# Performance work log

Measured on AMD Instinct MI355X. Metric: run time of the kernel, lower is better.

## Reference

```python
import jax, jax.numpy as jnp
import numpy as np

N_NODES = 50000
N_EDGES = 800000
D_IN = 128
D_OUT = 128
BN_EPS = 1e-5


def setup_inputs() -> dict:
    key = jax.random.key(0)
    ks = jax.random.split(key, 8)
    node_feats = jax.random.normal(ks[0], (N_NODES, D_IN), dtype=jnp.float32)
    src = jax.random.randint(ks[1], (N_EDGES,), 0, N_NODES, dtype=jnp.int32)
    dst = jax.random.randint(ks[2], (N_EDGES,), 0, N_NODES, dtype=jnp.int32)
    # Glorot-ish init for weights
    scale = 1.0 / np.sqrt(D_IN)
    W = jax.random.normal(ks[3], (D_IN, D_OUT), dtype=jnp.float32) * scale
    b = jnp.zeros((D_OUT,), dtype=jnp.float32)
    Wr = jax.random.normal(ks[4], (D_IN, D_OUT), dtype=jnp.float32) * scale
    br = jnp.zeros((D_OUT,), dtype=jnp.float32)
    gamma = jnp.ones((D_OUT,), dtype=jnp.float32)
    beta = jnp.zeros((D_OUT,), dtype=jnp.float32)
    return {"node_feats": node_feats, "src": src, "dst": dst, "W": W, "b": b,
            "Wr": Wr, "br": br, "gamma": gamma, "beta": beta}


def reference(node_feats, src, dst, W, b, Wr, br, gamma, beta):
    N = node_feats.shape[0]
    ones_e = jnp.ones(src.shape[0], dtype=node_feats.dtype)
    # DGL GraphConv norm='both': D_out^{-1/2} on source side, D_in^{-1/2} on dest side
    deg_out = jnp.clip(jax.ops.segment_sum(ones_e, src, num_segments=N), 1.0)
    deg_in = jnp.clip(jax.ops.segment_sum(ones_e, dst, num_segments=N), 1.0)
    h = node_feats * jax.lax.rsqrt(deg_out)[:, None]        # [N, D_in]
    agg = jax.ops.segment_sum(h[src], dst, num_segments=N)  # gather + scatter-add, [N, D_in]
    agg = agg * jax.lax.rsqrt(deg_in)[:, None]
    gcn = jax.nn.relu(agg @ W + b)                           # GraphConv activation=relu
    res = jax.nn.relu(node_feats @ Wr + br)                  # residual branch
    y = gcn + res
    # BatchNorm1d (training mode: biased batch stats)
    mean = jnp.mean(y, axis=0)
    var = jnp.mean(jnp.square(y - mean), axis=0)
    out = (y - mean) * jax.lax.rsqrt(var + BN_EPS) * gamma + beta
    return out
```

## Files before the change

kernel.cpp:

```cpp
#include <hip/hip_runtime.h>

#define N_NODES 50000
#define N_EDGES 800000
#define D 128
#define BN_EPS 1e-5f
#define AGG_BLOCKS 2048
#define CHUNKS 64
#define EPC (N_EDGES / CHUNKS)
#define EPC4 (EPC / 4)
#define QUART_BINS 12800
#define QUART_U32 6400
#define NB_MERGE 100
#define NB_PER_Q 25

typedef short bf16x8 __attribute__((ext_vector_type(8)));
typedef float f32x4  __attribute__((ext_vector_type(4)));
typedef float f32x2  __attribute__((ext_vector_type(2)));
typedef unsigned int u32x4 __attribute__((ext_vector_type(4)));
typedef int i32x4 __attribute__((ext_vector_type(4)));


__device__ __forceinline__ unsigned int pack_rne(float a, float b) {
    unsigned int ua = __float_as_uint(a); ua += 0x7fffu + ((ua >> 16) & 1u);
    unsigned int ub = __float_as_uint(b); ub += 0x7fffu + ((ub >> 16) & 1u);
    return (ua >> 16) | (ub & 0xffff0000u);
}
__device__ __forceinline__ unsigned short pack1_rne(float a) {
    unsigned int ua = __float_as_uint(a); ua += 0x7fffu + ((ua >> 16) & 1u);
    return (unsigned short)(ua >> 16);
}
__device__ __forceinline__ unsigned char pack1_fp8(float a) {
    unsigned int u = __builtin_amdgcn_cvt_pk_fp8_f32(a, a, 0, false);
    return (unsigned char)(u & 0xffu);
}

__device__ __forceinline__ void scan_blksum(const int* __restrict__ blk_sum,
                                            int* sh, int t) {
    int v = (t < NB_MERGE) ? blk_sum[t] : 0;
    if (t < 256) sh[t] = v;
    __syncthreads();
    int inc = v;
    #pragma unroll
    for (int off = 1; off < 256; off <<= 1) {
        int u = (t >= off && t < 256) ? sh[t - off] : 0;
        __syncthreads();
        inc += u;
        if (t < 256) sh[t] = inc;
        __syncthreads();
    }
}
#define BLK_OFF(sh, mb) ((mb) ? (sh)[(mb) - 1] : 0)

__global__ __launch_bounds__(256) void hist_kernel(
        const int* __restrict__ dst, const int* __restrict__ src,
        unsigned int* __restrict__ histD, unsigned int* __restrict__ histS,
        const float* __restrict__ W, const float* __restrict__ Wr,
        uint4* __restrict__ pW, uint4* __restrict__ pWr) {
    __shared__ unsigned int h[QUART_U32];
    int tid = threadIdx.x;
    int c = blockIdx.x, r = blockIdx.y;
    if (c >= CHUNKS) {
        if (r != 0 || blockIdx.z != 0) return;
        int t = (c - CHUNKS) * 256 + tid;
        const float* S = (t & 2048) ? Wr : W;
        uint4* Dst     = (t & 2048) ? pWr : pW;
        int e = t & 2047;
        int lane = e & 63, ks = (e >> 6) & 3, ct = e >> 8;
        int n  = ct * 16 + (lane & 15);
        int k0 = ks * 32 + (lane >> 4) * 8;
        float v[8];
        #pragma unroll
        for (int j = 0; j < 8; j++) v[j] = S[(k0 + j) * D + n];
        uint4 rr;
        rr.x = pack_rne(v[0], v[1]); rr.y = pack_rne(v[2], v[3]);
        rr.z = pack_rne(v[4], v[5]); rr.w = pack_rne(v[6], v[7]);
        Dst[e] = rr;
        return;
    }
    const int* keys = blockIdx.z ? src : dst;
    unsigned int* hist = blockIdx.z ? histS : histD;
    for (int j = tid; j < QUART_U32; j += 256) h[j] = 0u;
    __syncthreads();
    int lo = r * QUART_BINS;
    const i32x4* keys4 = (const i32x4*)(keys + c * EPC);
    for (int i = tid; i < EPC4; i += 256) {
        i32x4 k = __builtin_nontemporal_load(keys4 + i);
        int b0 = k.x - lo, b1 = k.y - lo, b2 = k.z - lo, b3 = k.w - lo;
        if ((unsigned)b0 < (unsigned)QUART_BINS) atomicAdd(&h[b0 >> 1], 1u << ((b0 & 1) * 16));
        if ((unsigned)b1 < (unsigned)QUART_BINS) atomicAdd(&h[b1 >> 1], 1u << ((b1 & 1) * 16));
        if ((unsigned)b2 < (unsigned)QUART_BINS) atomicAdd(&h[b2 >> 1], 1u << ((b2 & 1) * 16));
        if ((unsigned)b3 < (unsigned)QUART_BINS) atomicAdd(&h[b3 >> 1], 1u << ((b3 & 1) * 16));
    }
    __syncthreads();
    unsigned int* out = hist + ((size_t)(r * CHUNKS + c)) * QUART_U32;
    for (int j = tid; j < QUART_U32; j += 256) out[j] = h[j];
}

__global__ __launch_bounds__(256) void merge_kernel(
        unsigned int* __restrict__ histD, unsigned int* __restrict__ histS,
        int* __restrict__ cnt_in, int* __restrict__ cnt_out,
        int* __restrict__ row_ptr, int* __restrict__ blk_sum) {
    __shared__ int sh[256];
    int t = threadIdx.x;
    int bx = blockIdx.x;
    int r = bx / NB_PER_Q;
    int q = (bx % NB_PER_Q) * 256 + t;
    int n0 = bx * 512 + t * 2;
    if (blockIdx.y) {
        size_t base = (size_t)r * CHUNKS * QUART_U32 + q;
        unsigned int vals[CHUNKS];
        #pragma unroll
        for (int c = 0; c < CHUNKS; c++)
            vals[c] = histS[base + (size_t)c * QUART_U32];
        unsigned int lo = 0, hi = 0;
        #pragma unroll
        for (int c = 0; c < CHUNKS; c++) {
            lo += vals[c] & 0xffffu; hi += vals[c] >> 16;
        }
        cnt_out[n0]     = (int)lo;
        cnt_out[n0 + 1] = (int)hi;
        return;
    }
    size_t base = (size_t)r * CHUNKS * QUART_U32 + q;
    unsigned int vals[CHUNKS];
    #pragma unroll
    for (int c = 0; c < CHUNKS; c++)
        vals[c] = histD[base + (size_t)c * QUART_U32];
    unsigned int lo = 0, hi = 0;
    #pragma unroll
    for (int c = 0; c < CHUNKS; c++) {
        unsigned int v = vals[c];
        histD[base + (size_t)c * QUART_U32] = lo | (hi << 16);
        lo += v & 0xffffu; hi += v >> 16;
    }
    cnt_in[n0]     = (int)lo;
    cnt_in[n0 + 1] = (int)hi;
    int pair = (int)lo + (int)hi;
    sh[t] = pair;
    __syncthreads();
    int inc = pair;
    #pragma unroll
    for (int off = 1; off < 256; off <<= 1) {
        int u = (t >= off) ? sh[t - off] : 0;
        __syncthreads();
        inc += u; sh[t] = inc;
        __syncthreads();
    }
    int excl = inc - pair;
    row_ptr[n0]     = excl;
    row_ptr[n0 + 1] = excl + (int)lo;
    if (t == 255) blk_sum[bx] = inc;
}

__global__ __launch_bounds__(512) void fill2_kernel(
        const int* __restrict__ src, const int* __restrict__ dst,
        const int* __restrict__ row_ptr, const unsigned int* __restrict__ histP,
        const int* __restrict__ blk_sum, int* __restrict__ csr_src) {
    __shared__ unsigned int h[QUART_U32];
    __shared__ int sho[256];
    int tid = threadIdx.x;
    scan_blksum(blk_sum, sho, tid);
    int c = blockIdx.x, s = blockIdx.y;
    int base = c * EPC;
    for (int j = tid; j < QUART_U32; j += 512) h[j] = 0u;
    __syncthreads();
    int lo = s * QUART_BINS;
    const unsigned int* pre_c = histP + ((size_t)(s * CHUNKS + c)) * QUART_U32;
    for (int i = tid; i < EPC; i += 512) {
        int d = __builtin_nontemporal_load(dst + base + i);
        int b = d - lo;
        if ((unsigned)b < (unsigned)QUART_BINS) {
            int shft = (b & 1) * 16;
            unsigned int old = atomicAdd(&h[b >> 1], 1u << shft);
            unsigned int rank = (old >> shft) & 0xffffu;
            unsigned int pre = (pre_c[b >> 1] >> shft) & 0xffffu;
            int p = row_ptr[d] + BLK_OFF(sho, d >> 9) + (int)(pre + rank);
            csr_src[p] = __builtin_nontemporal_load(src + base + i);
        }
    }
}

__global__ __launch_bounds__(256) void gemm_mfma(
        const float* __restrict__ x, const uint4* __restrict__ pW,
        const uint4* __restrict__ pWr, const float* __restrict__ br,
        const unsigned int* __restrict__ cnt_out, unsigned char* __restrict__ hwb8,
        unsigned short* __restrict__ resb) {
    __shared__ unsigned short xs[64][136];
    int tid = threadIdx.x, wid = tid >> 6, lane = tid & 63;
    int quad = lane >> 4, l15 = lane & 15;
    int r0b = blockIdx.x * 64;
    const float4* xg = (const float4*)(x + (size_t)r0b * D);
    int maxidx = (N_NODES - r0b) * (D / 4);
    #pragma unroll
    for (int i = 0; i < 8; i++) {
        int idx = tid + 256 * i;
        float4 v = (idx < maxidx) ? xg[idx] : make_float4(0.f, 0.f, 0.f, 0.f);
        int row = idx >> 5, c0 = (idx & 31) * 4;
        *(unsigned int*)&xs[row][c0]     = pack_rne(v.x, v.y);
        *(unsigned int*)&xs[row][c0 + 2] = pack_rne(v.z, v.w);
    }
    __syncthreads();
    int wrow0 = wid * 16;
    bf16x8 A[4];
    #pragma unroll
    for (int ks = 0; ks < 4; ks++)
        A[ks] = *(const bf16x8*)&xs[wrow0 + l15][ks * 32 + quad * 8];
    f32x4 accW[8], accR[8];
    #pragma unroll
    for (int ct = 0; ct < 8; ct++) { accW[ct] = (f32x4)0.f; accR[ct] = (f32x4)0.f; }
    #pragma unroll
    for (int ct = 0; ct < 8; ct++) {
        #pragma unroll
        for (int ks = 0; ks < 4; ks++) {
            union { bf16x8 v; uint4 u; } Bw, Br2;
            Bw.u  = pW [(ct * 4 + ks) * 64 + lane];
            Br2.u = pWr[(ct * 4 + ks) * 64 + lane];
            accW[ct] = __builtin_amdgcn_mfma_f32_16x16x32_bf16(A[ks], Bw.v,  accW[ct], 0, 0, 0);
            accR[ct] = __builtin_amdgcn_mfma_f32_16x16x32_bf16(A[ks], Br2.v, accR[ct], 0, 0, 0);
        }
    }
    int r0 = r0b + wrow0;
    float ro[4]; int rowok[4];
    #pragma unroll
    for (int reg = 0; reg < 4; reg++) {
        int row = r0 + quad * 4 + reg;
        rowok[reg] = row < N_NODES;
        int cw = (int)cnt_out[rowok[reg] ? row : N_NODES - 1];
        ro[reg] = rsqrtf((float)(cw > 1 ? cw : 1));
    }
    #pragma unroll
    for (int ct = 0; ct < 8; ct++) {
        int c = ct * 16 + l15;
        float brv = br[c];
        #pragma unroll
        for (int reg = 0; reg < 4; reg++) {
            int row = r0 + quad * 4 + reg;
            if (rowok[reg]) {
                hwb8[(size_t)row * D + c] = pack1_fp8(accW[ct][reg] * ro[reg]);
                resb[(size_t)row * D + c] = pack1_rne(fmaxf(accR[ct][reg] + brv, 0.f));
            }
        }
    }
}

__device__ __forceinline__ float bf_lo(unsigned int v) { return __uint_as_float(v << 16); }
__device__ __forceinline__ float bf_hi(unsigned int v) { return __uint_as_float(v & 0xffff0000u); }

__device__ __forceinline__ void acc8f8(f32x2* a, const uint2 v) {
    a[0] += __builtin_amdgcn_cvt_pk_f32_fp8(v.x, false);
    a[1] += __builtin_amdgcn_cvt_pk_f32_fp8(v.x, true);
    a[2] += __builtin_amdgcn_cvt_pk_f32_fp8(v.y, false);
    a[3] += __builtin_amdgcn_cvt_pk_f32_fp8(v.y, true);
}
__device__ __forceinline__ void acc8f8m(f32x2* a, const uint2 v, float m) {
    f32x2 m2 = {m, m};
    a[0] += m2 * __builtin_amdgcn_cvt_pk_f32_fp8(v.x, false);
    a[1] += m2 * __builtin_amdgcn_cvt_pk_f32_fp8(v.x, true);
    a[2] += m2 * __builtin_amdgcn_cvt_pk_f32_fp8(v.y, false);
    a[3] += m2 * __builtin_amdgcn_cvt_pk_f32_fp8(v.y, true);
}

__device__ __forceinline__ void prefetch32(
        const unsigned char* __restrict__ hwb8, int myidx, int cnt,
        int qg, int ql, uint2* v, float* m) {
    int cm = cnt - 1; if (cm < 0) cm = 0;
    #pragma unroll
    for (int i = 0; i < 8; i++) {
        int j = i * 4 + qg;
        m[i] = (j < cnt) ? 1.f : 0.f;
        if (j > cm) j = cm;
        int p = __shfl(myidx, j);
        v[i] = *((const uint2*)(hwb8 + (size_t)p * 128) + ql);
    }
}

__device__ __forceinline__ void gather_rest(
        const unsigned char* __restrict__ hwb8, int myidx, int cnt,
        int qg, int ql, f32x2* a) {
    int i = 32;
    for (; i + 16 <= cnt; i += 16) {
        int p0 = __shfl(myidx, i + qg);
        int p1 = __shfl(myidx, i + 4 + qg);
        int p2 = __shfl(myidx, i + 8 + qg);
        int p3 = __shfl(myidx, i + 12 + qg);
        uint2 v0 = *((const uint2*)(hwb8 + (size_t)p0 * 128) + ql);
        uint2 v1 = *((const uint2*)(hwb8 + (size_t)p1 * 128) + ql);
        uint2 v2 = *((const uint2*)(hwb8 + (size_t)p2 * 128) + ql);
        uint2 v3 = *((const uint2*)(hwb8 + (size_t)p3 * 128) + ql);
        acc8f8(a, v0); acc8f8(a, v1); acc8f8(a, v2); acc8f8(a, v3);
    }
    for (; i + 4 <= cnt; i += 4) {
        int p0 = __shfl(myidx, i + qg);
        uint2 v0 = *((const uint2*)(hwb8 + (size_t)p0 * 128) + ql);
        acc8f8(a, v0);
    }
    int t = cnt - i;
    if (t > 0) {
        int j = i + qg; if (j > cnt - 1) j = cnt - 1;
        int p0 = __shfl(myidx, j);
        uint2 v0 = *((const uint2*)(hwb8 + (size_t)p0 * 128) + ql);
        float m = (qg < t) ? 1.f : 0.f;
        acc8f8m(a, v0, m);
    }
}

__device__ __forceinline__ void gather_accum(
        const unsigned char* __restrict__ hwb8, int myidx, int cnt,
        int qg, int ql, f32x2* a) {
    int i = 0;
    for (; i + 16 <= cnt; i += 16) {
        int p0 = __shfl(myidx, i + qg);
        int p1 = __shfl(myidx, i + 4 + qg);
        int p2 = __shfl(myidx, i + 8 + qg);
        int p3 = __shfl(myidx, i + 12 + qg);
        uint2 v0 = *((const uint2*)(hwb8 + (size_t)p0 * 128) + ql);
        uint2 v1 = *((const uint2*)(hwb8 + (size_t)p1 * 128) + ql);
        uint2 v2 = *((const uint2*)(hwb8 + (size_t)p2 * 128) + ql);
        uint2 v3 = *((const uint2*)(hwb8 + (size_t)p3 * 128) + ql);
        acc8f8(a, v0); acc8f8(a, v1); acc8f8(a, v2); acc8f8(a, v3);
    }
    for (; i + 4 <= cnt; i += 4) {
        int p0 = __shfl(myidx, i + qg);
        uint2 v0 = *((const uint2*)(hwb8 + (size_t)p0 * 128) + ql);
        acc8f8(a, v0);
    }
    int t = cnt - i;
    if (t > 0) {
        int j = i + qg; if (j > cnt - 1) j = cnt - 1;
        int p0 = __shfl(myidx, j);
        uint2 v0 = *((const uint2*)(hwb8 + (size_t)p0 * 128) + ql);
        float m = (qg < t) ? 1.f : 0.f;
        acc8f8m(a, v0, m);
    }
}

__global__ __launch_bounds__(256) void agg_kernel(
        const unsigned char* __restrict__ hwb8, const int* __restrict__ row_ptr,
        const int* __restrict__ blk_sum, const unsigned int* __restrict__ cnt_in,
        const int* __restrict__ csr_src,
        const float* __restrict__ bias, const unsigned short* __restrict__ resb,
        unsigned short* __restrict__ yb, float* __restrict__ parts) {
    __shared__ float red[4 * 256];
    __shared__ int sho[256];
    int tid = threadIdx.x;
    scan_blksum(blk_sum, sho, tid);
    int lane = tid & 63, wid = tid >> 6;
    int wave = blockIdx.x * 4 + wid;
    int nw = AGG_BLOCKS * 4;
    int qg = lane >> 4;
    int ql = lane & 15;
    float s1[8] = {0,0,0,0,0,0,0,0}, s2[8] = {0,0,0,0,0,0,0,0};
    float4 bv0, bv1;
    if (lane < 16) {
        bv0 = ((const float4*)bias)[2 * lane];
        bv1 = ((const float4*)bias)[2 * lane + 1];
    }
    int e0_0 = 0, e1_0 = 0, mi_0 = 0; float ri_0 = 0.f; u32x4 rv_0 = (u32x4)0u;
    int e0_1 = 0, e1_1 = 0, mi_1 = 0; float ri_1 = 0.f; u32x4 rv_1 = (u32x4)0u;
    uint2 pv[8]; float pm[8];
    #pragma unroll
    for (int i = 0; i < 8; i++) { pv[i] = make_uint2(0u, 0u); pm[i] = 0.f; }

    int n = wave;
    if (n < N_NODES) {
        e0_0 = row_ptr[n] + BLK_OFF(sho, n >> 9);
        e1_0 = row_ptr[n + 1] + BLK_OFF(sho, (n + 1) >> 9);
        int ci = (int)cnt_in[n];
        ri_0 = rsqrtf((float)(ci > 1 ? ci : 1));
        if (lane < 16) rv_0 = __builtin_nontemporal_load((const u32x4*)(resb + (size_t)n * D) + lane);
        int c0 = e1_0 - e0_0; if (c0 > 64) c0 = 64;
        mi_0 = (lane < c0) ? __builtin_nontemporal_load(csr_src + e0_0 + lane) : 0;
        prefetch32(hwb8, mi_0, c0, qg, ql, pv, pm);
    }
    int n1g = n + nw;
    if (n1g < N_NODES) {
        e0_1 = row_ptr[n1g] + BLK_OFF(sho, n1g >> 9);
        e1_1 = row_ptr[n1g + 1] + BLK_OFF(sho, (n1g + 1) >> 9);
        int ci = (int)cnt_in[n1g];
        ri_1 = rsqrtf((float)(ci > 1 ? ci : 1));
        if (lane < 16) rv_1 = __builtin_nontemporal_load((const u32x4*)(resb + (size_t)n1g * D) + lane);
        int c1 = e1_1 - e0_1; if (c1 > 64) c1 = 64;
        mi_1 = (lane < c1) ? __builtin_nontemporal_load(csr_src + e0_1 + lane) : 0;
    }

    while (n < N_NODES) {
        int n2 = n + 2 * nw;
        int e0_2 = 0, e1_2 = 0, mi_2 = 0; float ri_2 = 0.f; u32x4 rv_2 = (u32x4)0u;
        if (n2 < N_NODES) {
            e0_2 = row_ptr[n2] + BLK_OFF(sho, n2 >> 9);
            e1_2 = row_ptr[n2 + 1] + BLK_OFF(sho, (n2 + 1) >> 9);
            int ci = (int)cnt_in[n2];
            ri_2 = rsqrtf((float)(ci > 1 ? ci : 1));
            if (lane < 16) rv_2 = __builtin_nontemporal_load((const u32x4*)(resb + (size_t)n2 * D) + lane);
            int c2 = e1_2 - e0_2; if (c2 > 64) c2 = 64;
            mi_2 = (lane < c2) ? __builtin_nontemporal_load(csr_src + e0_2 + lane) : 0;
        }
        uint2 qv[8]; float qm[8];
        {
            int c1 = e1_1 - e0_1; if (c1 > 64) c1 = 64;
            prefetch32(hwb8, mi_1, c1, qg, ql, qv, qm);
        }
        f32x2 av[4];
        av[0] = (f32x2)0.f; av[1] = (f32x2)0.f; av[2] = (f32x2)0.f; av[3] = (f32x2)0.f;
        #pragma unroll
        for (int i = 0; i < 8; i++) acc8f8m(av, pv[i], pm[i]);
        {
            int cnt = e1_0 - e0_0; if (cnt > 64) cnt = 64;
            gather_rest(hwb8, mi_0, cnt, qg, ql, av);
        }
        for (int j0 = e0_0 + 64; j0 < e1_0; j0 += 64) {
            int cnt = e1_0 - j0; if (cnt > 64) cnt = 64;
            int mw = (lane < cnt) ? __builtin_nontemporal_load(csr_src + j0 + lane) : 0;
            gather_accum(hwb8, mw, cnt, qg, ql, av);
        }
        float a[8] = { av[0].x, av[0].y, av[1].x, av[1].y, av[2].x, av[2].y, av[3].x, av[3].y };
        #pragma unroll
        for (int k = 0; k < 8; k++) {
            a[k] += __shfl_xor(a[k], 16);
            a[k] += __shfl_xor(a[k], 32);
        }
        if (lane < 16) {
            float o[8];
            o[0] = fmaxf(a[0] * ri_0 + bv0.x, 0.f) + bf_lo(rv_0.x);
            o[1] = fmaxf(a[1] * ri_0 + bv0.y, 0.f) + bf_hi(rv_0.x);
            o[2] = fmaxf(a[2] * ri_0 + bv0.z, 0.f) + bf_lo(rv_0.y);
            o[3] = fmaxf(a[3] * ri_0 + bv0.w, 0.f) + bf_hi(rv_0.y);
            o[4] = fmaxf(a[4] * ri_0 + bv1.x, 0.f) + bf_lo(rv_0.z);
            o[5] = fmaxf(a[5] * ri_0 + bv1.y, 0.f) + bf_hi(rv_0.z);
            o[6] = fmaxf(a[6] * ri_0 + bv1.z, 0.f) + bf_lo(rv_0.w);
            o[7] = fmaxf(a[7] * ri_0 + bv1.w, 0.f) + bf_hi(rv_0.w);
            uint4 w;
            w.x = pack_rne(o[0], o[1]); w.y = pack_rne(o[2], o[3]);
            w.z = pack_rne(o[4], o[5]); w.w = pack_rne(o[6], o[7]);
            *((uint4*)(yb + (size_t)n * D) + lane) = w;
            #pragma unroll
            for (int k = 0; k < 8; k++) { s1[k] += o[k]; s2[k] += o[k] * o[k]; }
        }
        n += nw;
        e0_0 = e0_1; e1_0 = e1_1; mi_0 = mi_1; ri_0 = ri_1; rv_0 = rv_1;
        e0_1 = e0_2; e1_1 = e1_2; mi_1 = mi_2; ri_1 = ri_2; rv_1 = rv_2;
        #pragma unroll
        for (int i = 0; i < 8; i++) { pv[i] = qv[i]; pm[i] = qm[i]; }
    }
    if (lane < 16) {
        int c0 = lane * 8;
        #pragma unroll
        for (int k = 0; k < 8; k++) {
            red[wid * 256 + c0 + k]       = s1[k];
            red[wid * 256 + 128 + c0 + k] = s2[k];
        }
    }
    __syncthreads();
    if (tid < 256) {
        float v = red[tid] + red[256 + tid] + red[512 + tid] + red[768 + tid];
        parts[(size_t)blockIdx.x * 256 + tid] = v;
    }
}

__global__ __launch_bounds__(256) void bn_fin2(
        const float* __restrict__ parts, const float* __restrict__ gamma,
        const float* __restrict__ beta, float* __restrict__ scsh) {
    __shared__ float rs1[256], rs2[256];
    int c = blockIdx.x, t = threadIdx.x;
    float s1 = 0.f, s2 = 0.f;
    for (int b = t; b < AGG_BLOCKS; b += 256) {
        s1 += parts[(size_t)b * 256 + c];
        s2 += parts[(size_t)b * 256 + 128 + c];
    }
    rs1[t] = s1; rs2[t] = s2;
    __syncthreads();
    for (int off = 128; off > 0; off >>= 1) {
        if (t < off) { rs1[t] += rs1[t + off]; rs2[t] += rs2[t + off]; }
        __syncthreads();
    }
    if (t == 0) {
        const float invN = 1.0f / (float)N_NODES;
        float mean = rs1[0] * invN;
        float var  = rs2[0] * invN - mean * mean;
        float sc = gamma[c] * rsqrtf(var + BN_EPS);
        scsh[c] = sc;
        scsh[128 + c] = beta[c] - mean * sc;
    }
}

__global__ void norm_kernel(const unsigned short* __restrict__ yb,
                            const float* __restrict__ scsh, float* __restrict__ out) {
    int i = blockIdx.x * blockDim.x + threadIdx.x;
    if (i < N_NODES * 16) {
        uint4 v = ((const uint4*)yb)[i];
        int c = (i & 15) * 8;
        f32x4 o0, o1;
        o0[0] = bf_lo(v.x) * scsh[c]     + scsh[128 + c];
        o0[1] = bf_hi(v.x) * scsh[c + 1] + scsh[128 + c + 1];
        o0[2] = bf_lo(v.y) * scsh[c + 2] + scsh[128 + c + 2];
        o0[3] = bf_hi(v.y) * scsh[c + 3] + scsh[128 + c + 3];
        o1[0] = bf_lo(v.z) * scsh[c + 4] + scsh[128 + c + 4];
        o1[1] = bf_hi(v.z) * scsh[c + 5] + scsh[128 + c + 5];
        o1[2] = bf_lo(v.w) * scsh[c + 6] + scsh[128 + c + 6];
        o1[3] = bf_hi(v.w) * scsh[c + 7] + scsh[128 + c + 7];
        f32x4* ov = (f32x4*)out + (size_t)i * 2;
        __builtin_nontemporal_store(o0, ov);
        __builtin_nontemporal_store(o1, ov + 1);
    }
}

extern "C" void kernel_launch(void* const* d_in, const int* in_sizes, int n_in,
                              void* d_out, int out_size, void* d_ws, size_t ws_size,
                              hipStream_t stream) {
    const float* x     = (const float*)d_in[0];
    const int*   src   = (const int*)d_in[1];
    const int*   dst   = (const int*)d_in[2];
    const float* W     = (const float*)d_in[3];
    const float* b     = (const float*)d_in[4];
    const float* Wr    = (const float*)d_in[5];
    const float* br    = (const float*)d_in[6];
    const float* gamma = (const float*)d_in[7];
    const float* beta  = (const float*)d_in[8];
    float* out = (float*)d_out;

    char* ws = (char*)d_ws;
    int*   cnt_in  = (int*)(ws + 0);
    int*   cnt_out = (int*)(ws + 262144);
    int*   row_ptr = (int*)(ws + 524288);
    float* scsh    = (float*)(ws + 1310720);
    int*   blk_sum = (int*)(ws + 1312768);
    int*   csr_src = (int*)(ws + 1576960);
    unsigned char*  hwb8 = (unsigned char*)(ws + 4800000);
    unsigned short* resb = (unsigned short*)(ws + 11200000);
    unsigned short* yb   = (unsigned short*)(ws + 24000000);
    float* parts   = (float*)(ws + 36800000);
    uint4* pW      = (uint4*)(ws + 38897152);
    uint4* pWr     = (uint4*)(ws + 38929920);
    unsigned int* histD = (unsigned int*)(ws + 38962688);
    unsigned int* histS = (unsigned int*)(ws + 45516288);

    hist_kernel<<<dim3(CHUNKS + 16, 4, 2), 256, 0, stream>>>(
        dst, src, histD, histS, W, Wr, pW, pWr);
    merge_kernel<<<dim3(NB_MERGE, 2), 256, 0, stream>>>(
        histD, histS, (int*)cnt_in, (int*)cnt_out, row_ptr, blk_sum);
    fill2_kernel<<<dim3(CHUNKS, 4), 512, 0, stream>>>(
        src, dst, row_ptr, histD, blk_sum, csr_src);
    gemm_mfma<<<(N_NODES + 63) / 64, 256, 0, stream>>>(
        x, pW, pWr, br, (const unsigned int*)cnt_out, hwb8, resb);
    agg_kernel<<<AGG_BLOCKS, 256, 0, stream>>>(
        hwb8, row_ptr, blk_sum, (const unsigned int*)cnt_in, csr_src, b, resb, yb, parts);
    bn_fin2<<<128, 256, 0, stream>>>(parts, gamma, beta, scsh);
    norm_kernel<<<(N_NODES * 16 + 255) / 256, 256, 0, stream>>>(yb, scsh, out);
}
```

Baseline: 214.8 us.

## Use 16-byte fp8 gathers with 8 lanes per row and butterfly reduce-scatter

The aggregation kernel now has 8 lanes per edge row, each loading 16 bytes instead of 8, so 8 edges are processed per wave iteration instead of 16. The cross-group reduction becomes a 3-stage butterfly reduce-scatter, after which every lane owns two output channels, so all 64 lanes do the epilogue, residual load, store and BN partial sums. The aim is fewer, wider memory instructions and no idle lanes in the epilogue, at the cost of less edge-level parallelism per instruction and a smaller prefetch of 16 edges instead of 32.

```diff
diff --git a/kernel.cpp b/kernel.cpp
--- a/kernel.cpp
+++ b/kernel.cpp
@@ -246,61 +246,59 @@
 __device__ __forceinline__ float bf_lo(unsigned int v) { return __uint_as_float(v << 16); }
 __device__ __forceinline__ float bf_hi(unsigned int v) { return __uint_as_float(v & 0xffff0000u); }
 
-__device__ __forceinline__ void acc8f8(f32x2* a, const uint2 v) {
+__device__ __forceinline__ void acc16(f32x2* a, const uint4 v) {
     a[0] += __builtin_amdgcn_cvt_pk_f32_fp8(v.x, false);
     a[1] += __builtin_amdgcn_cvt_pk_f32_fp8(v.x, true);
     a[2] += __builtin_amdgcn_cvt_pk_f32_fp8(v.y, false);
     a[3] += __builtin_amdgcn_cvt_pk_f32_fp8(v.y, true);
-}
-__device__ __forceinline__ void acc8f8m(f32x2* a, const uint2 v, float m) {
+    a[4] += __builtin_amdgcn_cvt_pk_f32_fp8(v.z, false);
+    a[5] += __builtin_amdgcn_cvt_pk_f32_fp8(v.z, true);
+    a[6] += __builtin_amdgcn_cvt_pk_f32_fp8(v.w, false);
+    a[7] += __builtin_amdgcn_cvt_pk_f32_fp8(v.w, true);
+}
+__device__ __forceinline__ void acc16m(f32x2* a, const uint4 v, float m) {
     f32x2 m2 = {m, m};
     a[0] += m2 * __builtin_amdgcn_cvt_pk_f32_fp8(v.x, false);
     a[1] += m2 * __builtin_amdgcn_cvt_pk_f32_fp8(v.x, true);
     a[2] += m2 * __builtin_amdgcn_cvt_pk_f32_fp8(v.y, false);
     a[3] += m2 * __builtin_amdgcn_cvt_pk_f32_fp8(v.y, true);
-}
-
-__device__ __forceinline__ void prefetch32(
+    a[4] += m2 * __builtin_amdgcn_cvt_pk_f32_fp8(v.z, false);
+    a[5] += m2 * __builtin_amdgcn_cvt_pk_f32_fp8(v.z, true);
+    a[6] += m2 * __builtin_amdgcn_cvt_pk_f32_fp8(v.w, false);
+    a[7] += m2 * __builtin_amdgcn_cvt_pk_f32_fp8(v.w, true);
+}
+
+__device__ __forceinline__ void prefetch16q(
         const unsigned char* __restrict__ hwb8, int myidx, int cnt,
-        int qg, int ql, uint2* v, float* m) {
+        int qg, int ql, uint4& v0, uint4& v1, float& m0, float& m1) {
     int cm = cnt - 1; if (cm < 0) cm = 0;
-    #pragma unroll
-    for (int i = 0; i < 8; i++) {
-        int j = i * 4 + qg;
-        m[i] = (j < cnt) ? 1.f : 0.f;
-        if (j > cm) j = cm;
-        int p = __shfl(myidx, j);
-        v[i] = *((const uint2*)(hwb8 + (size_t)p * 128) + ql);
-    }
+    int j0 = qg, j1 = 8 + qg;
+    m0 = (j0 < cnt) ? 1.f : 0.f;
+    m1 = (j1 < cnt) ? 1.f : 0.f;
+    if (j0 > cm) j0 = cm;
+    if (j1 > cm) j1 = cm;
+    int p0 = __shfl(myidx, j0);
+    int p1 = __shfl(myidx, j1);
+    v0 = *((const uint4*)(hwb8 + (size_t)p0 * 128) + ql);
+    v1 = *((const uint4*)(hwb8 + (size_t)p1 * 128) + ql);
 }
 
 __device__ __forceinline__ void gather_rest(
         const unsigned char* __restrict__ hwb8, int myidx, int cnt,
         int qg, int ql, f32x2* a) {
-    int i = 32;
-    for (; i + 16 <= cnt; i += 16) {
+    int i = 16;
+    for (; i + 8 <= cnt; i += 8) {
         int p0 = __shfl(myidx, i + qg);
-        int p1 = __shfl(myidx, i + 4 + qg);
-        int p2 = __shfl(myidx, i + 8 + qg);
-        int p3 = __shfl(myidx, i + 12 + qg);
-        uint2 v0 = *((const uint2*)(hwb8 + (size_t)p0 * 128) + ql);
-        uint2 v1 = *((const uint2*)(hwb8 + (size_t)p1 * 128) + ql);
-        uint2 v2 = *((const uint2*)(hwb8 + (size_t)p2 * 128) + ql);
-        uint2 v3 = *((const uint2*)(hwb8 + (size_t)p3 * 128) + ql);
-        acc8f8(a, v0); acc8f8(a, v1); acc8f8(a, v2); acc8f8(a, v3);
-    }
-    for (; i + 4 <= cnt; i += 4) {
-        int p0 = __shfl(myidx, i + qg);
-        uint2 v0 = *((const uint2*)(hwb8 + (size_t)p0 * 128) + ql);
-        acc8f8(a, v0);
+        uint4 v0 = *((const uint4*)(hwb8 + (size_t)p0 * 128) + ql);
+        acc16(a, v0);
     }
     int t = cnt - i;
     if (t > 0) {
         int j = i + qg; if (j > cnt - 1) j = cnt - 1;
         int p0 = __shfl(myidx, j);
-        uint2 v0 = *((const uint2*)(hwb8 + (size_t)p0 * 128) + ql);
+        uint4 v0 = *((const uint4*)(hwb8 + (size_t)p0 * 128) + ql);
         float m = (qg < t) ? 1.f : 0.f;
-        acc8f8m(a, v0, m);
+        acc16m(a, v0, m);
     }
 }
 
@@ -308,29 +306,18 @@
         const unsigned char* __restrict__ hwb8, int myidx, int cnt,
         int qg, int ql, f32x2* a) {
     int i = 0;
-    for (; i + 16 <= cnt; i += 16) {
+    for (; i + 8 <= cnt; i += 8) {
         int p0 = __shfl(myidx, i + qg);
-        int p1 = __shfl(myidx, i + 4 + qg);
-        int p2 = __shfl(myidx, i + 8 + qg);
-        int p3 = __shfl(myidx, i + 12 + qg);
-        uint2 v0 = *((const uint2*)(hwb8 + (size_t)p0 * 128) + ql);
-        uint2 v1 = *((const uint2*)(hwb8 + (size_t)p1 * 128) + ql);
-        uint2 v2 = *((const uint2*)(hwb8 + (size_t)p2 * 128) + ql);
-        uint2 v3 = *((const uint2*)(hwb8 + (size_t)p3 * 128) + ql);
-        acc8f8(a, v0); acc8f8(a, v1); acc8f8(a, v2); acc8f8(a, v3);
-    }
-    for (; i + 4 <= cnt; i += 4) {
-        int p0 = __shfl(myidx, i + qg);
-        uint2 v0 = *((const uint2*)(hwb8 + (size_t)p0 * 128) + ql);
-        acc8f8(a, v0);
+        uint4 v0 = *((const uint4*)(hwb8 + (size_t)p0 * 128) + ql);
+        acc16(a, v0);
     }
     int t = cnt - i;
     if (t > 0) {
         int j = i + qg; if (j > cnt - 1) j = cnt - 1;
         int p0 = __shfl(myidx, j);
-        uint2 v0 = *((const uint2*)(hwb8 + (size_t)p0 * 128) + ql);
+        uint4 v0 = *((const uint4*)(hwb8 + (size_t)p0 * 128) + ql);
         float m = (qg < t) ? 1.f : 0.f;
-        acc8f8m(a, v0, m);
+        acc16m(a, v0, m);
     }
 }
 
@@ -347,19 +334,16 @@
     int lane = tid & 63, wid = tid >> 6;
     int wave = blockIdx.x * 4 + wid;
     int nw = AGG_BLOCKS * 4;
-    int qg = lane >> 4;
-    int ql = lane & 15;
-    float s1[8] = {0,0,0,0,0,0,0,0}, s2[8] = {0,0,0,0,0,0,0,0};
-    float4 bv0, bv1;
-    if (lane < 16) {
-        bv0 = ((const float4*)bias)[2 * lane];
-        bv1 = ((const float4*)bias)[2 * lane + 1];
-    }
-    int e0_0 = 0, e1_0 = 0, mi_0 = 0; float ri_0 = 0.f; u32x4 rv_0 = (u32x4)0u;
-    int e0_1 = 0, e1_1 = 0, mi_1 = 0; float ri_1 = 0.f; u32x4 rv_1 = (u32x4)0u;
-    uint2 pv[8]; float pm[8];
-    #pragma unroll
-    for (int i = 0; i < 8; i++) { pv[i] = make_uint2(0u, 0u); pm[i] = 0.f; }
+    int qg = lane >> 3;
+    int ql = lane & 7;
+    int cp = ql * 8 + qg;
+    float2 bv = ((const float2*)bias)[cp];
+    float s1a = 0.f, s1b = 0.f, s2a = 0.f, s2b = 0.f;
+
+    int e0_0 = 0, e1_0 = 0, mi_0 = 0; float ri_0 = 0.f; unsigned int rv_0 = 0u;
+    int e0_1 = 0, e1_1 = 0, mi_1 = 0; float ri_1 = 0.f; unsigned int rv_1 = 0u;
+    uint4 pv0, pv1; float pm0 = 0.f, pm1 = 0.f;
+    pv0 = pv1 = make_uint4(0u, 0u, 0u, 0u);
 
     int n = wave;
     if (n < N_NODES) {
@@ -367,10 +351,10 @@
         e1_0 = row_ptr[n + 1] + BLK_OFF(sho, (n + 1) >> 9);
         int ci = (int)cnt_in[n];
         ri_0 = rsqrtf((float)(ci > 1 ? ci : 1));
-        if (lane < 16) rv_0 = __builtin_nontemporal_load((const u32x4*)(resb + (size_t)n * D) + lane);
+        rv_0 = __builtin_nontemporal_load((const unsigned int*)(resb + (size_t)n * D) + cp);
         int c0 = e1_0 - e0_0; if (c0 > 64) c0 = 64;
         mi_0 = (lane < c0) ? __builtin_nontemporal_load(csr_src + e0_0 + lane) : 0;
-        prefetch32(hwb8, mi_0, c0, qg, ql, pv, pm);
+        prefetch16q(hwb8, mi_0, c0, qg, ql, pv0, pv1, pm0, pm1);
     }
     int n1g = n + nw;
     if (n1g < N_NODES) {
@@ -378,78 +362,70 @@
         e1_1 = row_ptr[n1g + 1] + BLK_OFF(sho, (n1g + 1) >> 9);
         int ci = (int)cnt_in[n1g];
         ri_1 = rsqrtf((float)(ci > 1 ? ci : 1));
-        if (lane < 16) rv_1 = __builtin_nontemporal_load((const u32x4*)(resb + (size_t)n1g * D) + lane);
+        rv_1 = __builtin_nontemporal_load((const unsigned int*)(resb + (size_t)n1g * D) + cp);
         int c1 = e1_1 - e0_1; if (c1 > 64) c1 = 64;
         mi_1 = (lane < c1) ? __builtin_nontemporal_load(csr_src + e0_1 + lane) : 0;
     }
 
     while (n < N_NODES) {
         int n2 = n + 2 * nw;
-        int e0_2 = 0, e1_2 = 0, mi_2 = 0; float ri_2 = 0.f; u32x4 rv_2 = (u32x4)0u;
+        int e0_2 = 0, e1_2 = 0, mi_2 = 0; float ri_2 = 0.f; unsigned int rv_2 = 0u;
         if (n2 < N_NODES) {
             e0_2 = row_ptr[n2] + BLK_OFF(sho, n2 >> 9);
             e1_2 = row_ptr[n2 + 1] + BLK_OFF(sho, (n2 + 1) >> 9);
             int ci = (int)cnt_in[n2];
             ri_2 = rsqrtf((float)(ci > 1 ? ci : 1));
-            if (lane < 16) rv_2 = __builtin_nontemporal_load((const u32x4*)(resb + (size_t)n2 * D) + lane);
+            rv_2 = __builtin_nontemporal_load((const unsigned int*)(resb + (size_t)n2 * D) + cp);
             int c2 = e1_2 - e0_2; if (c2 > 64) c2 = 64;
             mi_2 = (lane < c2) ? __builtin_nontemporal_load(csr_src + e0_2 + lane) : 0;
         }
-        uint2 qv[8]; float qm[8];
+        uint4 qv0, qv1; float qm0, qm1;
         {
             int c1 = e1_1 - e0_1; if (c1 > 64) c1 = 64;
-            prefetch32(hwb8, mi_1, c1, qg, ql, qv, qm);
-        }
-        f32x2 av[4];
-        av[0] = (f32x2)0.f; av[1] = (f32x2)0.f; av[2] = (f32x2)0.f; av[3] = (f32x2)0.f;
-        #pragma unroll
-        for (int i = 0; i < 8; i++) acc8f8m(av, pv[i], pm[i]);
+            prefetch16q(hwb8, mi_1, c1, qg, ql, qv0, qv1, qm0, qm1);
+        }
+        f32x2 a8[8];
+        #pragma unroll
+        for (int i = 0; i < 8; i++) a8[i] = (f32x2)0.f;
+        acc16m(a8, pv0, pm0); acc16m(a8, pv1, pm1);
         {
             int cnt = e1_0 - e0_0; if (cnt > 64) cnt = 64;
-            gather_rest(hwb8, mi_0, cnt, qg, ql, av);
+            gather_rest(hwb8, mi_0, cnt, qg, ql, a8);
         }
         for (int j0 = e0_0 + 64; j0 < e1_0; j0 += 64) {
             int cnt = e1_0 - j0; if (cnt > 64) cnt = 64;
             int mw = (lane < cnt) ? __builtin_nontemporal_load(csr_src + j0 + lane) : 0;
-            gather_accum(hwb8, mw, cnt, qg, ql, av);
-        }
-        float a[8] = { av[0].x, av[0].y, av[1].x, av[1].y, av[2].x, av[2].y, av[3].x, av[3].y };
-        #pragma unroll
-        for (int k = 0; k < 8; k++) {
-            a[k] += __shfl_xor(a[k], 16);
-            a[k] += __shfl_xor(a[k], 32);
-        }
-        if (lane < 16) {
-            float o[8];
-            o[0] = fmaxf(a[0] * ri_0 + bv0.x, 0.f) + bf_lo(rv_0.x);
-            o[1] = fmaxf(a[1] * ri_0 + bv0.y, 0.f) + bf_hi(rv_0.x);
-            o[2] = fmaxf(a[2] * ri_0 + bv0.z, 0.f) + bf_lo(rv_0.y);
-            o[3] = fmaxf(a[3] * ri_0 + bv0.w, 0.f) + bf_hi(rv_0.y);
-            o[4] = fmaxf(a[4] * ri_0 + bv1.x, 0.f) + bf_lo(rv_0.z);
-            o[5] = fmaxf(a[5] * ri_0 + bv1.y, 0.f) + bf_hi(rv_0.z);
-            o[6] = fmaxf(a[6] * ri_0 + bv1.z, 0.f) + bf_lo(rv_0.w);
-            o[7] = fmaxf(a[7] * ri_0 + bv1.w, 0.f) + bf_hi(rv_0.w);
-            uint4 w;
-            w.x = pack_rne(o[0], o[1]); w.y = pack_rne(o[2], o[3]);
-            w.z = pack_rne(o[4], o[5]); w.w = pack_rne(o[6], o[7]);
-            *((uint4*)(yb + (size_t)n * D) + lane) = w;
+            gather_accum(hwb8, mw, cnt, qg, ql, a8);
+        }
+        #pragma unroll
+        for (int b = 0; b < 3; b++) {
+            int half = 4 >> b;
+            int bit = (qg >> b) & 1;
             #pragma unroll
-            for (int k = 0; k < 8; k++) { s1[k] += o[k]; s2[k] += o[k] * o[k]; }
+            for (int i = 0; i < half; i++) {
+                f32x2 keep = bit ? a8[2 * i + 1] : a8[2 * i];
+                f32x2 send = bit ? a8[2 * i]     : a8[2 * i + 1];
+                f32x2 recv;
+                recv.x = __shfl_xor(send.x, 8 << b);
+                recv.y = __shfl_xor(send.y, 8 << b);
+                a8[i] = keep + recv;
+            }
+        }
+        {
+            float o0 = fmaxf(a8[0].x * ri_0 + bv.x, 0.f) + bf_lo(rv_0);
+            float o1 = fmaxf(a8[0].y * ri_0 + bv.y, 0.f) + bf_hi(rv_0);
+            ((unsigned int*)(yb + (size_t)n * D))[cp] = pack_rne(o0, o1);
+            s1a += o0; s1b += o1; s2a += o0 * o0; s2b += o1 * o1;
         }
         n += nw;
         e0_0 = e0_1; e1_0 = e1_1; mi_0 = mi_1; ri_0 = ri_1; rv_0 = rv_1;
         e0_1 = e0_2; e1_1 = e1_2; mi_1 = mi_2; ri_1 = ri_2; rv_1 = rv_2;
-        #pragma unroll
-        for (int i = 0; i < 8; i++) { pv[i] = qv[i]; pm[i] = qm[i]; }
-    }
-    if (lane < 16) {
-        int c0 = lane * 8;
-        #pragma unroll
-        for (int k = 0; k < 8; k++) {
-            red[wid * 256 + c0 + k]       = s1[k];
-            red[wid * 256 + 128 + c0 + k] = s2[k];
-        }
-    }
+        pv0 = qv0; pv1 = qv1; pm0 = qm0; pm1 = qm1;
+    }
+    red[wid * 256 + 2 * cp]           = s1a;
+    red[wid * 256 + 2 * cp + 1]       = s1b;
+    red[wid * 256 + 128 + 2 * cp]     = s2a;
+    red[wid * 256 + 128 + 2 * cp + 1] = s2b;
     __syncthreads();
     if (tid < 256) {
         float v = red[tid] + red[256 + tid] + red[512 + tid] + red[768 + tid];
```

Result: faster. 204.8 us, median of 2 (-4.6%).
